# Performance work log

Hardware: AMD Instinct MI355X
Metric: run time of the kernel (lower is better)

The kernel has to match this reference:

```python
import jax, jax.numpy as jnp
import numpy as np

L = 2          # loopnum
BS = 64        # batch
T = 512        # tracklength
EC = 1024      # ecnum
CA1 = 1024     # ca1num
CA3 = 1024     # ca3num
ACT = 2        # actnum
TS = 0.1
SIGMA = 5.0    # ca3sigma


def setup_inputs() -> dict:
    key = jax.random.key(0)
    ks = jax.random.split(key, 10)
    return {
        "cue_ec3input": jax.random.normal(ks[0], (BS, T, EC), dtype=jnp.float32),
        "ec3_last": jax.random.uniform(ks[1], (L, BS, EC), dtype=jnp.float32),
        "ec5_last": jax.random.uniform(ks[2], (L, BS, EC), dtype=jnp.float32),
        "ca1_last": jax.random.uniform(ks[3], (L, BS, CA1), dtype=jnp.float32),
        # per-loop parameters, stacked on leading loop axis (mirrors nn.ModuleList)
        "wca3ca1": jax.random.uniform(ks[4], (L, CA3, CA1), dtype=jnp.float32) * 0.01,
        "wec3ca1": jax.random.normal(ks[5], (L, EC, CA1), dtype=jnp.float32) * 0.03,   # ~xavier scale
        "wca1ec5": jax.random.normal(ks[6], (L, CA1, EC), dtype=jnp.float32) * 0.03,
        "ca1bias": jnp.zeros((L, CA1), dtype=jnp.float32),
        "ec5bias": jnp.zeros((L, EC), dtype=jnp.float32),
        # interLayer i: nn.Linear(ca1num, ecnum) -> weight (EC, CA1), bias (EC,)
        "inter_w": jax.random.normal(ks[7], (L, EC, CA1), dtype=jnp.float32) * 0.02,
        "inter_b": jnp.zeros((L, EC), dtype=jnp.float32),
        "wca1act": jax.random.normal(ks[8], (CA1, ACT), dtype=jnp.float32) * 0.03,
        "actbias": jnp.zeros((ACT,), dtype=jnp.float32),
    }


def reference(cue_ec3input, ec3_last, ec5_last, ca1_last,
              wca3ca1, wec3ca1, wca1ec5, ca1bias, ec5bias,
              inter_w, inter_b, wca1act, actbias):
    ca3center = jnp.linspace(0.0, float(T), CA3)          # (CA3,)
    positions = jnp.arange(T, dtype=jnp.float32)          # (T,)
    cue_t = jnp.swapaxes(cue_ec3input, 0, 1)              # (T, BS, EC)

    def step(carry, xin):
        ec3, ec5, ca1 = carry                             # each (L, BS, dim)
        x, cue_x = xin                                    # scalar, (BS, EC)
        ca3 = jnp.exp(-(ca3center - x) ** 2 / (2.0 * SIGMA ** 2))  # (CA3,)
        ec3input = cue_x
        new_ec3, new_ec5, new_ca1 = [], [], []
        for i in range(L):                                # fixed, structurally distinct loops
            ca1_i = jax.nn.relu(
                jax.nn.sigmoid(10.0 * (ca3 @ wca3ca1[i] - 0.5))           # (CA1,)
                * (1.0 + 3.0 * jax.nn.sigmoid(ec3[i] @ wec3ca1[i]))       # (BS, CA1)
                - ca1bias[i]
            )
            ec5_i = ec5[i] + 10.0 * TS * (ca1_i @ wca1ec5[i]) + ec5bias[i]
            ec5_i = 0.69 + 0.3 * jax.nn.sigmoid(4.0 * (ec5_i - 0.3))
            ec3_i = ec5_i * ec3[i] + 0.6 * ec3input
            ec3input = ca1_i @ inter_w[i].T + inter_b[i]  # feed next loop
            new_ec3.append(ec3_i); new_ec5.append(ec5_i); new_ca1.append(ca1_i)
        ec3 = jnp.stack(new_ec3); ec5 = jnp.stack(new_ec5); ca1 = jnp.stack(new_ca1)
        # histories record batch element 0 only, as in the original
        hist = (ec3[:, 0, :], ec5[:, 0, :], ca1[:, 0, :])
        return (ec3, ec5, ca1), hist

    (ec3, ec5, ca1), (ec3his, ec5his, ca1his) = jax.lax.scan(
        step, (ec3_last, ec5_last, ca1_last), (positions, cue_t))

    # scan stacks on axis 0 -> (T, L, dim); original layout is (L, T, dim)
    ec3his = jnp.swapaxes(ec3his, 0, 1)
    ec5his = jnp.swapaxes(ec5his, 0, 1)
    ca1his = jnp.swapaxes(ca1his, 0, 1)

    actCell = ca1[-1] @ wca1act + actbias                 # (BS, ACT)
    return actCell, ec3his, ec5his, ca1his
```

## Files before the change

### kernel.cpp

```cpp
#include <hip/hip_runtime.h>

#define Lnum 2
#define BSn  64
#define Tn   512
#define ECn  1024
#define CA1n 1024
#define CHUNK 16

typedef short bf16x8 __attribute__((ext_vector_type(8)));
typedef float f32x4  __attribute__((ext_vector_type(4)));

#define MFMA16(a,b,c) __builtin_amdgcn_mfma_f32_16x16x32_bf16((a),(b),(c),0,0,0)

#define OUT_E3  128
#define OUT_E5  (128 + Lnum*Tn*ECn)
#define OUT_CA1 (128 + 2*Lnum*Tn*ECn)

#define WS_FLAGS 0
#define WS_EC3S  8192
#define WS_CA1S  4202496
#define WS_EC5F  8396800
#define WS_EC3F  8921088
#define WS_CA1L  9445376
#define WS_S     9707520
#define WS_W1T   11804672
#define WS_W2T   15998976
#define WS_W3T   20193280

#define AST(p, v) __hip_atomic_store((p), (v), __ATOMIC_RELAXED, __HIP_MEMORY_SCOPE_AGENT)
#define ALD(p)    __hip_atomic_load((p), __ATOMIC_RELAXED, __HIP_MEMORY_SCOPE_AGENT)

__device__ __forceinline__ float sigm(float x) { return 1.0f / (1.0f + __expf(-x)); }

__device__ __forceinline__ unsigned f2bfu(float f) {
  unsigned u = __float_as_uint(f);
  u += 0x7fffu + ((u >> 16) & 1u);
  return u >> 16;
}
__device__ __forceinline__ short f2bf(float f) { return (short)f2bfu(f); }
__device__ __forceinline__ float bf2f(short s) {
  return __uint_as_float(((unsigned)(unsigned short)s) << 16);
}

__device__ __forceinline__ void pollGE(const unsigned* s, unsigned need) {
  const int lane = threadIdx.x & 63;
  while (__any(ALD(&s[lane]) < need)) {}
  __builtin_amdgcn_sched_barrier(0);
  asm volatile("" ::: "memory");
}
__device__ __forceinline__ void publish(unsigned* s, int bid, unsigned val) {
  asm volatile("s_waitcnt vmcnt(0)" ::: "memory");
  __syncthreads();
  if (threadIdx.x == 0) AST(&s[bid], val);
}


__global__ void prep_state(const float* __restrict__ ec3_last,
                           const float* __restrict__ ec5_last,
                           unsigned* __restrict__ flags, unsigned* __restrict__ ec3su,
                           float* __restrict__ ec5f, float* __restrict__ ec3f) {
  int i = blockIdx.x * blockDim.x + threadIdx.x;
  if (i < 2048) flags[i] = 0u;
  float v3 = ec3_last[i];
  ec3f[i] = v3;
  ec5f[i] = ec5_last[i];
  if (i < Lnum * BSn * 512) {
    float lo = ec3_last[2 * i], hi = ec3_last[2 * i + 1];
    ec3su[15 * 65536 + i] = f2bfu(lo) | (f2bfu(hi) << 16);
  }
}

__global__ void prep_wt(const float* __restrict__ w1, const float* __restrict__ w2,
                        short* __restrict__ w1t, short* __restrict__ w2t) {
  __shared__ float tile[64][65];
  const int b = blockIdx.x;
  const int m  = b >> 9;
  const int li = (b >> 8) & 1;
  const int kt = (b >> 4) & 15;
  const int ct = b & 15;
  const float* src = (m == 0 ? w1 : w2) + li * (1024 * 1024);
  short* dst = (m == 0 ? w1t : w2t) + li * (1024 * 1024);
#pragma unroll
  for (int i = 0; i < 16; ++i) {
    int idx = threadIdx.x + i * 256;
    int r = idx >> 6, c = idx & 63;
    tile[r][c] = src[(kt * 64 + r) * 1024 + ct * 64 + c];
  }
  __syncthreads();
#pragma unroll
  for (int i = 0; i < 16; ++i) {
    int idx = threadIdx.x + i * 256;
    int c = idx >> 6, r = idx & 63;
    dst[(ct * 64 + c) * 1024 + kt * 64 + r] = f2bf(tile[r][c]);
  }
}

__global__ void prep_w3(const float* __restrict__ inter_w, short* __restrict__ w3t) {
  int i = blockIdx.x * blockDim.x + threadIdx.x;
  w3t[i] = f2bf(inter_w[i]);
}

__global__ void prep_ca3(const float* __restrict__ wca3ca1, short* __restrict__ S) {
  const int t = blockIdx.x >> 1, li = blockIdx.x & 1;
  __shared__ float gauss[192];
  const float stepc = 512.0f / 1023.0f;
  const float tf = (float)t;
  int kmin = (int)floorf((tf - 40.0f) / stepc) - 1; if (kmin < 0) kmin = 0;
  int kmax = (int)ceilf((tf + 40.0f) / stepc) + 1;  if (kmax > 1023) kmax = 1023;
  int nw = kmax - kmin + 1;
  for (int j = threadIdx.x; j < nw; j += 256) {
    float d = (float)(kmin + j) * stepc - tf;
    gauss[j] = __expf(-d * d * 0.02f);
  }
  __syncthreads();
  const float* W = wca3ca1 + li * (1024 * 1024);
  for (int c = threadIdx.x; c < 1024; c += 256) {
    float s = 0.0f;
    for (int j = 0; j < nw; ++j) s += gauss[j] * W[(kmin + j) * 1024 + c];
    S[(li * Tn + t) * 1024 + c] = f2bf(sigm(10.0f * (s - 0.5f)));
  }
}

__global__ void __launch_bounds__(256, 1) stepchunk(
    const float* __restrict__ cue,
    const short* __restrict__ w1t, const short* __restrict__ w2t,
    const short* __restrict__ w3t, const short* __restrict__ stab,
    const float* __restrict__ ca1bias, const float* __restrict__ ec5bias,
    const float* __restrict__ interb,
    unsigned* __restrict__ flags, short* __restrict__ ec3s,
    short* __restrict__ ca1s, float* __restrict__ ec5f, float* __restrict__ ec3f,
    float* __restrict__ ca1l, float* __restrict__ out, int t0) {
  extern __shared__ short lds[];
  short* BT1 = lds;
  short* BT2 = lds + 16 * 1024;
  short* BT3 = lds + 32 * 1024;

  unsigned* sentA = flags;
  unsigned* sentB = flags + 128;
  unsigned* ec3su = (unsigned*)ec3s;
  unsigned* ca1su = (unsigned*)ca1s;

  const int b = blockIdx.x;
  const int li = b >> 6;
  const int c0 = (b & 63) << 4;
  const int tid = threadIdx.x;
  const int lane = tid & 63, wave = tid >> 6;
  const int fr = lane & 15, ks = lane >> 4;
  const int r0 = wave << 4;
  const int ccol = c0 + fr;

  {
    int cp = tid & 15;
    int k0 = (tid >> 4) << 6;
    int xm = (cp & 7) << 3;
    const short* s1 = w1t + li * 1048576 + (c0 + cp) * 1024;
    const short* s2 = w2t + li * 1048576 + (c0 + cp) * 1024;
#pragma unroll
    for (int j = 0; j < 8; ++j) {
      int k = k0 + j * 8;
      *(bf16x8*)(BT1 + cp * 1024 + (k ^ xm)) = *(const bf16x8*)(s1 + k);
      *(bf16x8*)(BT2 + cp * 1024 + (k ^ xm)) = *(const bf16x8*)(s2 + k);
    }
    if (li == 1) {
      const short* s3 = w3t + (c0 + cp) * 1024;
#pragma unroll
      for (int j = 0; j < 8; ++j) {
        int k = k0 + j * 8;
        *(bf16x8*)(BT3 + cp * 1024 + (k ^ xm)) = *(const bf16x8*)(s3 + k);
      }
    }
  }
  __syncthreads();

  const int xsw = (fr & 7) << 3;
  const short* B1 = BT1 + fr * 1024;
  const short* B2 = BT2 + fr * 1024;
  const short* B3 = BT3 + fr * 1024;

  const float cb  = ca1bias[li * 1024 + ccol];
  const float e5b = ec5bias[li * 1024 + ccol];
  const float ib0 = interb[1024 + ccol];

  float e5r[4], e3r[4];
#pragma unroll
  for (int r = 0; r < 4; ++r) {
    int sidx = li * 65536 + (r0 + ks * 4 + r) * 1024 + ccol;
    e5r[r] = ec5f[sidx];
    e3r[r] = ec3f[sidx];
  }

  bf16x8 ar[32], ar3[32];

  for (int tt = 0; tt < CHUNK; ++tt) {
    const int t = t0 + tt;
    const int rd = (tt + 15) & 15;

    float cueq[4];
    if (li == 0) {
#pragma unroll
      for (int r = 0; r < 4; ++r)
        cueq[r] = cue[((r0 + ks * 4 + r) * Tn + t) * 1024 + ccol];
    }

    {
      pollGE(sentB + li * 64, (unsigned)t);
      const short* A1 = ec3s + ((rd * 2 + li) * 64 + (r0 + fr)) * 1024 + ks * 8;
#pragma unroll
      for (int kk = 0; kk < 16; ++kk) {
        ar[kk]      = *(const bf16x8*)(A1 + kk * 32);
        ar[16 + kk] = *(const bf16x8*)(A1 + 512 + kk * 32);
      }
      __builtin_amdgcn_sched_barrier(0);
      f32x4 a0 = {0.f,0.f,0.f,0.f}, a1 = {0.f,0.f,0.f,0.f};
#pragma unroll
      for (int kk = 0; kk < 16; ++kk) {
        a0 = MFMA16(ar[kk],      *(const bf16x8*)(B1 + ((kk * 32 + ks * 8) ^ xsw)),       a0);
        a1 = MFMA16(ar[16 + kk], *(const bf16x8*)(B1 + ((512 + kk * 32 + ks * 8) ^ xsw)), a1);
      }
      f32x4 acc = a0 + a1;
      const float g = bf2f(stab[(li * Tn + t) * 1024 + ccol]);
#pragma unroll
      for (int r = 0; r < 4; ++r) {
        int grow = r0 + ks * 4 + r;
        float cv = fmaxf(g * (1.0f + 3.0f * sigm(acc[r])) - cb, 0.0f);
        unsigned my = f2bfu(cv);
        unsigned pr = (unsigned)__shfl_xor((int)my, 1);
        if ((fr & 1) == 0)
          AST(ca1su + ((tt * 2 + li) * 64 + grow) * 512 + ((c0 + fr) >> 1), my | (pr << 16));
        if (grow == 0) out[OUT_CA1 + (li * Tn + t) * 1024 + ccol] = cv;
        if (t == Tn - 1 && li == 1) ca1l[grow * 1024 + ccol] = cv;
      }
      publish(sentA, b, (unsigned)(t + 1));
    }

    {
      pollGE(sentA + li * 64, (unsigned)(t + 1));
      if (li == 1) pollGE(sentA, (unsigned)(t + 1));
      const short* A2 = ca1s + ((tt * 2 + li) * 64 + (r0 + fr)) * 1024 + ks * 8;
#pragma unroll
      for (int kk = 0; kk < 16; ++kk) {
        ar[kk]      = *(const bf16x8*)(A2 + kk * 32);
        ar[16 + kk] = *(const bf16x8*)(A2 + 512 + kk * 32);
      }
      if (li == 1) {
        const short* A3 = ca1s + ((tt * 2) * 64 + (r0 + fr)) * 1024 + ks * 8;
#pragma unroll
        for (int kk = 0; kk < 16; ++kk) {
          ar3[kk]      = *(const bf16x8*)(A3 + kk * 32);
          ar3[16 + kk] = *(const bf16x8*)(A3 + 512 + kk * 32);
        }
      }
      __builtin_amdgcn_sched_barrier(0);
      f32x4 p0 = {0.f,0.f,0.f,0.f}, p1 = {0.f,0.f,0.f,0.f};
#pragma unroll
      for (int kk = 0; kk < 16; ++kk) {
        p0 = MFMA16(ar[kk],      *(const bf16x8*)(B2 + ((kk * 32 + ks * 8) ^ xsw)),       p0);
        p1 = MFMA16(ar[16 + kk], *(const bf16x8*)(B2 + ((512 + kk * 32 + ks * 8) ^ xsw)), p1);
      }
      f32x4 g2 = p0 + p1;

      f32x4 xin;
      if (li == 1) {
        f32x4 q0 = {0.f,0.f,0.f,0.f}, q1 = {0.f,0.f,0.f,0.f};
#pragma unroll
        for (int kk = 0; kk < 16; ++kk) {
          q0 = MFMA16(ar3[kk],      *(const bf16x8*)(B3 + ((kk * 32 + ks * 8) ^ xsw)),       q0);
          q1 = MFMA16(ar3[16 + kk], *(const bf16x8*)(B3 + ((512 + kk * 32 + ks * 8) ^ xsw)), q1);
        }
        f32x4 q = q0 + q1;
#pragma unroll
        for (int r = 0; r < 4; ++r) xin[r] = q[r] + ib0;
      } else {
#pragma unroll
        for (int r = 0; r < 4; ++r) xin[r] = cueq[r];
      }

#pragma unroll
      for (int r = 0; r < 4; ++r) {
        int grow = r0 + ks * 4 + r;
        float raw = e5r[r] + g2[r] + e5b;
        float e5 = 0.69f + 0.3f * sigm(4.0f * (raw - 0.3f));
        e5r[r] = e5;
        float e3 = e5 * e3r[r] + 0.6f * xin[r];
        e3r[r] = e3;
        unsigned my = f2bfu(e3);
        unsigned pr = (unsigned)__shfl_xor((int)my, 1);
        if ((fr & 1) == 0)
          AST(ec3su + ((tt * 2 + li) * 64 + grow) * 512 + ((c0 + fr) >> 1), my | (pr << 16));
        if (grow == 0) {
          out[OUT_E5 + (li * Tn + t) * 1024 + ccol] = e5;
          out[OUT_E3 + (li * Tn + t) * 1024 + ccol] = e3;
        }
      }
      publish(sentB, b, (unsigned)(t + 1));
    }
  }

#pragma unroll
  for (int r = 0; r < 4; ++r) {
    int sidx = li * 65536 + (r0 + ks * 4 + r) * 1024 + ccol;
    ec5f[sidx] = e5r[r];
    ec3f[sidx] = e3r[r];
  }
}

__global__ void act_cell(const float* __restrict__ ca1l, const float* __restrict__ wca1act,
                         const float* __restrict__ actbias, float* __restrict__ out) {
  int tid = threadIdx.x;
  if (tid < 128) {
    int b = tid >> 1, a = tid & 1;
    float s = 0.0f;
    for (int k = 0; k < 1024; ++k) s += ca1l[b * 1024 + k] * wca1act[k * 2 + a];
    out[b * 2 + a] = s + actbias[a];
  }
}

extern "C" void kernel_launch(void* const* d_in, const int* in_sizes, int n_in,
                              void* d_out, int out_size, void* d_ws, size_t ws_size,
                              hipStream_t stream) {
  (void)in_sizes; (void)n_in; (void)out_size; (void)ws_size;
  const float* cue      = (const float*)d_in[0];
  const float* ec3_last = (const float*)d_in[1];
  const float* ec5_last = (const float*)d_in[2];
  const float* wca3ca1  = (const float*)d_in[4];
  const float* wec3ca1  = (const float*)d_in[5];
  const float* wca1ec5  = (const float*)d_in[6];
  const float* ca1bias  = (const float*)d_in[7];
  const float* ec5bias  = (const float*)d_in[8];
  const float* inter_w  = (const float*)d_in[9];
  const float* inter_b  = (const float*)d_in[10];
  const float* wca1act  = (const float*)d_in[11];
  const float* actbias  = (const float*)d_in[12];
  float* out = (float*)d_out;

  char* ws = (char*)d_ws;
  unsigned* flags = (unsigned*)(ws + WS_FLAGS);
  short* ec3s = (short*)(ws + WS_EC3S);
  short* ca1s = (short*)(ws + WS_CA1S);
  float* ec5f = (float*)(ws + WS_EC5F);
  float* ec3f = (float*)(ws + WS_EC3F);
  float* ca1l = (float*)(ws + WS_CA1L);
  short* stab = (short*)(ws + WS_S);
  short* w1t  = (short*)(ws + WS_W1T);
  short* w2t  = (short*)(ws + WS_W2T);
  short* w3t  = (short*)(ws + WS_W3T);

  prep_state<<<dim3(512), dim3(256), 0, stream>>>(ec3_last, ec5_last, flags,
                                                  (unsigned*)ec3s, ec5f, ec3f);
  prep_wt<<<dim3(1024), dim3(256), 0, stream>>>(wec3ca1, wca1ec5, w1t, w2t);
  prep_w3<<<dim3(4096), dim3(256), 0, stream>>>(inter_w, w3t);
  prep_ca3<<<dim3(1024), dim3(256), 0, stream>>>(wca3ca1, stab);

  hipFuncSetAttribute((const void*)stepchunk,
                      hipFuncAttributeMaxDynamicSharedMemorySize, 98304);

  for (int c = 0; c < Tn / CHUNK; ++c) {
    stepchunk<<<dim3(128), dim3(256), 98304, stream>>>(
        cue, w1t, w2t, w3t, stab, ca1bias, ec5bias, inter_b,
        flags, ec3s, ca1s, ec5f, ec3f, ca1l, out, c * CHUNK);
  }

  act_cell<<<dim3(1), dim3(128), 0, stream>>>(ca1l, wca1act, actbias, out);
}
```

Measured before the change: 9.622 ms.

## Poll flags from one wave with sleep and defer history stores past publish

Only wave 0 spins on the cross-block flag arrays, with s_sleep in the loop, and the other waves wait at a block barrier. This cuts memory polling traffic and contention with the producing blocks. The two flag polls in loop 1 are merged into one combined wait. History stores and the final ca1 stores move after publish, so the flag goes out before those non-critical writes, and the cue load is issued before the wait to hide its latency. The risks are wakeup delay added by the sleep and an extra __syncthreads per phase on the serial critical path.

```diff
diff --git a/kernel.cpp b/kernel.cpp
--- a/kernel.cpp
+++ b/kernel.cpp
@@ -42,9 +42,16 @@
   return __uint_as_float(((unsigned)(unsigned short)s) << 16);
 }
 
-__device__ __forceinline__ void pollGE(const unsigned* s, unsigned need) {
+__device__ __forceinline__ void pollOne(const unsigned* s, unsigned need) {
   const int lane = threadIdx.x & 63;
-  while (__any(ALD(&s[lane]) < need)) {}
+  while (__any(ALD(&s[lane]) < need)) __builtin_amdgcn_s_sleep(2);
+  __builtin_amdgcn_sched_barrier(0);
+  asm volatile("" ::: "memory");
+}
+__device__ __forceinline__ void pollTwo(const unsigned* s, unsigned need) {
+  const int lane = threadIdx.x & 63;
+  while (__any((ALD(&s[lane]) < need) | (ALD(&s[64 + lane]) < need)))
+    __builtin_amdgcn_s_sleep(2);
   __builtin_amdgcn_sched_barrier(0);
   asm volatile("" ::: "memory");
 }
@@ -195,15 +202,10 @@
     const int t = t0 + tt;
     const int rd = (tt + 15) & 15;
 
-    float cueq[4];
-    if (li == 0) {
-#pragma unroll
-      for (int r = 0; r < 4; ++r)
-        cueq[r] = cue[((r0 + ks * 4 + r) * Tn + t) * 1024 + ccol];
-    }
-
+    f32x4 cvv;
     {
-      pollGE(sentB + li * 64, (unsigned)t);
+      if (wave == 0) pollOne(sentB + li * 64, (unsigned)t);
+      __syncthreads();
       const short* A1 = ec3s + ((rd * 2 + li) * 64 + (r0 + fr)) * 1024 + ks * 8;
 #pragma unroll
       for (int kk = 0; kk < 16; ++kk) {
@@ -223,19 +225,33 @@
       for (int r = 0; r < 4; ++r) {
         int grow = r0 + ks * 4 + r;
         float cv = fmaxf(g * (1.0f + 3.0f * sigm(acc[r])) - cb, 0.0f);
+        cvv[r] = cv;
         unsigned my = f2bfu(cv);
         unsigned pr = (unsigned)__shfl_xor((int)my, 1);
         if ((fr & 1) == 0)
           AST(ca1su + ((tt * 2 + li) * 64 + grow) * 512 + ((c0 + fr) >> 1), my | (pr << 16));
-        if (grow == 0) out[OUT_CA1 + (li * Tn + t) * 1024 + ccol] = cv;
-        if (t == Tn - 1 && li == 1) ca1l[grow * 1024 + ccol] = cv;
       }
       publish(sentA, b, (unsigned)(t + 1));
+#pragma unroll
+      for (int r = 0; r < 4; ++r) {
+        int grow = r0 + ks * 4 + r;
+        if (grow == 0) out[OUT_CA1 + (li * Tn + t) * 1024 + ccol] = cvv[r];
+        if (t == Tn - 1 && li == 1) ca1l[grow * 1024 + ccol] = cvv[r];
+      }
     }
 
     {
-      pollGE(sentA + li * 64, (unsigned)(t + 1));
-      if (li == 1) pollGE(sentA, (unsigned)(t + 1));
+      float cueq[4];
+      if (li == 0) {
+#pragma unroll
+        for (int r = 0; r < 4; ++r)
+          cueq[r] = cue[((r0 + ks * 4 + r) * Tn + t) * 1024 + ccol];
+      }
+      if (wave == 0) {
+        if (li == 0) pollOne(sentA, (unsigned)(t + 1));
+        else         pollTwo(sentA, (unsigned)(t + 1));
+      }
+      __syncthreads();
       const short* A2 = ca1s + ((tt * 2 + li) * 64 + (r0 + fr)) * 1024 + ks * 8;
 #pragma unroll
       for (int kk = 0; kk < 16; ++kk) {
@@ -277,22 +293,26 @@
 
 #pragma unroll
       for (int r = 0; r < 4; ++r) {
-        int grow = r0 + ks * 4 + r;
         float raw = e5r[r] + g2[r] + e5b;
         float e5 = 0.69f + 0.3f * sigm(4.0f * (raw - 0.3f));
         e5r[r] = e5;
         float e3 = e5 * e3r[r] + 0.6f * xin[r];
         e3r[r] = e3;
+        int grow = r0 + ks * 4 + r;
         unsigned my = f2bfu(e3);
         unsigned pr = (unsigned)__shfl_xor((int)my, 1);
         if ((fr & 1) == 0)
           AST(ec3su + ((tt * 2 + li) * 64 + grow) * 512 + ((c0 + fr) >> 1), my | (pr << 16));
+      }
+      publish(sentB, b, (unsigned)(t + 1));
+#pragma unroll
+      for (int r = 0; r < 4; ++r) {
+        int grow = r0 + ks * 4 + r;
         if (grow == 0) {
-          out[OUT_E5 + (li * Tn + t) * 1024 + ccol] = e5;
-          out[OUT_E3 + (li * Tn + t) * 1024 + ccol] = e3;
+          out[OUT_E5 + (li * Tn + t) * 1024 + ccol] = e5r[r];
+          out[OUT_E3 + (li * Tn + t) * 1024 + ccol] = e3r[r];
         }
       }
-      publish(sentB, b, (unsigned)(t + 1));
     }
   }
 
```

After: 8.965 ms. 1.07x faster.
